# Optimization experiments

Measured on AMD Instinct MI355X. Metric: run time of the kernel, lower is better.

## Reference

```python
import jax, jax.numpy as jnp
import numpy as np

N, E, D, H, C, HOPS = 50000, 1600000, 128, 4, 32, 3

def spectral_normalize(W, iters=5):
    # power iteration, fixed start vector (deterministic, jit-friendly)
    u = jnp.ones((W.shape[0],), W.dtype) / jnp.sqrt(jnp.float32(W.shape[0]))
    for _ in range(iters):
        v = W.T @ u; v = v / (jnp.linalg.norm(v) + 1e-12)
        u = W @ v;  u = u / (jnp.linalg.norm(u) + 1e-12)
    sigma = u @ (W @ v)
    return W / (sigma + 1e-12)

def layer_norm(x, g, b, eps=1e-5):
    m = jnp.mean(x, -1, keepdims=True)
    v = jnp.mean((x - m) ** 2, -1, keepdims=True)
    return (x - m) * jax.lax.rsqrt(v + eps) * g + b

def edge_softmax(logits, dst):
    # logits: [E, H]; softmax over edges sharing a destination node
    m = jax.ops.segment_max(logits, dst, num_segments=N)
    e = jnp.exp(logits - m[dst])
    s = jax.ops.segment_sum(e, dst, num_segments=N)
    return e / (s[dst] + 1e-16)

def gat_layer(h, src, dst, W, a_s, a_d, bias):
    xh = (h @ W).reshape(N, H, C)                      # [N,H,C]
    al_s = jnp.sum(xh * a_s, -1)                       # [N,H]
    al_d = jnp.sum(xh * a_d, -1)
    logits = jax.nn.leaky_relu(al_s[src] + al_d[dst], 0.2)  # [E,H]
    alpha = edge_softmax(logits, dst)                  # [E,H]
    msg = xh[src] * alpha[..., None]                   # [E,H,C]
    out = jax.ops.segment_sum(msg, dst, num_segments=N)
    return out.reshape(N, H * C) + bias

def ode_block(h, W_ode, b_ode, steps=4):
    # fixed-step RK4 over t in [0,1]; f(h) = gelu(h @ sn(W) + b)
    Wn = spectral_normalize(W_ode)
    f = lambda y: jax.nn.gelu(y @ Wn + b_ode, approximate=False)
    dt = 1.0 / steps
    def step(y, _):
        k1 = f(y); k2 = f(y + 0.5 * dt * k1)
        k3 = f(y + 0.5 * dt * k2); k4 = f(y + dt * k3)
        return y + (dt / 6.0) * (k1 + 2 * k2 + 2 * k3 + k4), None
    y, _ = jax.lax.scan(step, h, None, length=steps)
    return y

def multihop_broadcast(h, src, dst, att):
    deg = jnp.maximum(jax.ops.segment_sum(jnp.ones((E,), h.dtype), dst, num_segments=N), 1.0)
    hops = [h]
    cur = h
    for _ in range(HOPS):
        cur = jax.ops.segment_sum(cur[src], dst, num_segments=N) / deg[:, None]
        hops.append(cur)
    stack = jnp.stack(hops)                            # [HOPS+1, N, D]
    scores = jnp.einsum('knd,d->kn', stack, att)       # [HOPS+1, N]
    w = jax.nn.softmax(scores, axis=0)
    return jnp.einsum('kn,knd->nd', w, stack)

def encoder_fwd(x, edge_index, W_in, b_in, W1, a_src1, a_dst1, b1,
                W2, a_src2, a_dst2, b2, g1, be1, g2, be2, W_ode, b_ode, att):
    src, dst = edge_index[0], edge_index[1]
    h = jax.nn.gelu(x @ spectral_normalize(W_in) + b_in, approximate=False)
    h = layer_norm(jax.nn.gelu(gat_layer(h, src, dst, W1, a_src1, a_dst1, b1), approximate=False), g1, be1)
    h = layer_norm(jax.nn.gelu(gat_layer(h, src, dst, W2, a_src2, a_dst2, b2), approximate=False), g2, be2)
    h = ode_block(h, W_ode, b_ode)
    h = multihop_broadcast(h, src, dst, att)
    return h

def setup_inputs() -> dict:
    key = jax.random.key(0)
    ks = jax.random.split(key, 12)
    s = lambda d: 1.0 / np.sqrt(d)
    return {
        'x': jax.random.normal(ks[0], (N, D), jnp.float32),
        'edge_index': jax.random.randint(ks[1], (2, E), 0, N, jnp.int64),
        'W_in': jax.random.normal(ks[2], (D, D), jnp.float32) * s(D),
        'b_in': jnp.zeros((D,), jnp.float32),
        'W1': jax.random.normal(ks[3], (D, H * C), jnp.float32) * s(D),
        'a_src1': jax.random.normal(ks[4], (H, C), jnp.float32) * s(C),
        'a_dst1': jax.random.normal(ks[5], (H, C), jnp.float32) * s(C),
        'b1': jnp.zeros((H * C,), jnp.float32),
        'W2': jax.random.normal(ks[6], (D, H * C), jnp.float32) * s(D),
        'a_src2': jax.random.normal(ks[7], (H, C), jnp.float32) * s(C),
        'a_dst2': jax.random.normal(ks[8], (H, C), jnp.float32) * s(C),
        'b2': jnp.zeros((H * C,), jnp.float32),
        'g1': jnp.ones((D,), jnp.float32), 'be1': jnp.zeros((D,), jnp.float32),
        'g2': jnp.ones((D,), jnp.float32), 'be2': jnp.zeros((D,), jnp.float32),
        'W_ode': jax.random.normal(ks[9], (D, D), jnp.float32) * s(D),
        'b_ode': jnp.zeros((D,), jnp.float32),
        'att': jax.random.normal(ks[10], (D,), jnp.float32) * s(D),
    }

def reference(x, edge_index, W_in, b_in, W1, a_src1, a_dst1, b1, W2, a_src2, a_dst2, b2,
              g1, be1, g2, be2, W_ode, b_ode, att):
    return encoder_fwd(x, edge_index, W_in, b_in, W1, a_src1, a_dst1, b1,
                       W2, a_src2, a_dst2, b2, g1, be1, g2, be2, W_ode, b_ode, att)
```

## Files before the change

kernel.cpp:

```cpp
#include <hip/hip_runtime.h>
#include <math.h>


typedef __attribute__((ext_vector_type(8))) short bf16x8;
typedef __attribute__((ext_vector_type(4))) float f32x4;

#define BSN 256

__device__ __forceinline__ float gelu_f(float x) {
    return 0.5f * x * (1.0f + erff(x * 0.70710678118654752f));
}
__device__ __forceinline__ float gelu_sig(float x) {
    float y = 0.7978845608028654f * fmaf(0.044715f * x, x * x, x);
    float e = __expf(-2.0f * y);
    return x * __builtin_amdgcn_rcpf(1.0f + e);
}
__device__ __forceinline__ unsigned pack_bf16(float a, float b) {
    unsigned ua = __float_as_uint(a), ub = __float_as_uint(b);
    ua += 0x7fffu + ((ua >> 16) & 1u);
    ub += 0x7fffu + ((ub >> 16) & 1u);
    return (ua >> 16) | (ub & 0xffff0000u);
}
__device__ __forceinline__ unsigned short bfbits(float x) {
    unsigned u = __float_as_uint(x);
    u += 0x7fffu + ((u >> 16) & 1u);
    return (unsigned short)(u >> 16);
}
__device__ __forceinline__ float bf_lo(unsigned u) { return __uint_as_float(u << 16); }
__device__ __forceinline__ float bf_hi(unsigned u) { return __uint_as_float(u & 0xffff0000u); }
__device__ __forceinline__ int swz(int byte) { return byte ^ (((byte >> 8) & 15) << 4); }

__launch_bounds__(128, 1)
__global__ void sn_k(const float* __restrict__ Win, const float* __restrict__ Wode,
                     float* __restrict__ WnIn, float* __restrict__ WnOde)
{
    __shared__ float Ws[128 * 128];
    __shared__ float Wt[128 * 128];
    __shared__ float red[128];
    const float* W  = (blockIdx.x == 0) ? Win  : Wode;
    float*       Wn = (blockIdx.x == 0) ? WnIn : WnOde;
    const int t = threadIdx.x;

    for (int i = t * 4; i < 16384; i += 512) {
        float4 v = *(const float4*)&W[i];
        *(float4*)&Ws[i] = v;
        int r = i >> 7, c = i & 127;
        Wt[(c + 0) * 128 + r] = v.x;
        Wt[(c + 1) * 128 + r] = v.y;
        Wt[(c + 2) * 128 + r] = v.z;
        Wt[(c + 3) * 128 + r] = v.w;
    }
    __syncthreads();

    float u = 0.088388347648318447f;
    float v = 0.0f;
    for (int it = 0; it < 5; it++) {
        red[t] = u; __syncthreads();
        float vv = 0.f;
        for (int i = 0; i < 128; i++) vv = fmaf(Ws[i * 128 + t], red[i], vv);
        __syncthreads();
        red[t] = vv * vv; __syncthreads();
        for (int s = 64; s > 0; s >>= 1) { if (t < s) red[t] += red[t + s]; __syncthreads(); }
        float nv = sqrtf(red[0]) + 1e-12f;
        v = vv / nv;
        __syncthreads();
        red[t] = v; __syncthreads();
        float uu = 0.f;
        for (int i = 0; i < 128; i++) uu = fmaf(Wt[i * 128 + t], red[i], uu);
        __syncthreads();
        red[t] = uu * uu; __syncthreads();
        for (int s = 64; s > 0; s >>= 1) { if (t < s) red[t] += red[t + s]; __syncthreads(); }
        float nu = sqrtf(red[0]) + 1e-12f;
        u = uu / nu;
        __syncthreads();
    }
    red[t] = v; __syncthreads();
    float wv = 0.f;
    for (int i = 0; i < 128; i++) wv = fmaf(Wt[i * 128 + t], red[i], wv);
    __syncthreads();
    red[t] = u * wv; __syncthreads();
    for (int s = 64; s > 0; s >>= 1) { if (t < s) red[t] += red[t + s]; __syncthreads(); }
    float inv = 1.0f / (red[0] + 1e-12f);
    __syncthreads();
    for (int i = t * 4; i < 16384; i += 512) {
        float4 w = *(const float4*)&Ws[i];
        w.x *= inv; w.y *= inv; w.z *= inv; w.w *= inv;
        *(float4*)&Wn[i] = w;
    }
}

__global__ void hist_k(const int* __restrict__ dst, int* __restrict__ deg, int E, int N)
{
    int e = blockIdx.x * blockDim.x + threadIdx.x;
    if (e < E) {
        int d = dst[e];
        d = (d < 0) ? 0 : (d >= N ? N - 1 : d);
        atomicAdd(&deg[d], 1);
    }
}

__launch_bounds__(1024, 1)
__global__ void scan_k(const int* __restrict__ deg, int* __restrict__ offs, int n)
{
    __shared__ int part[1024];
    const int t = threadIdx.x;
    const int chunk = (n + 1023) >> 10;
    int lo = t * chunk; if (lo > n) lo = n;
    int hi = lo + chunk; if (hi > n) hi = n;
    int s = 0;
    for (int i = lo; i < hi; i++) s += deg[i];
    part[t] = s; __syncthreads();
    for (int d = 1; d < 1024; d <<= 1) {
        int v = (t >= d) ? part[t - d] : 0;
        __syncthreads();
        part[t] += v;
        __syncthreads();
    }
    int run = (t == 0) ? 0 : part[t - 1];
    for (int i = lo; i < hi; i++) { offs[i] = run; run += deg[i]; }
    if (t == 1023) offs[n] = run;
}

__global__ void binit_k(const int* __restrict__ offs, int* __restrict__ bcur, int N, int nb)
{
    int b = blockIdx.x * blockDim.x + threadIdx.x;
    if (b < nb) {
        int n = b * BSN; if (n > N) n = N;
        bcur[b] = offs[n];
    }
}

__launch_bounds__(256, 2)
__global__ void scatA_k(const int* __restrict__ src, const int* __restrict__ dst,
                        int* __restrict__ bcur, uint2* __restrict__ pairbuf, int E, int N)
{
    __shared__ int cnt[256];
    __shared__ int sc[256];
    __shared__ int ebase[256];
    __shared__ int delta[256];
    __shared__ uint2 pr[4096];
    __shared__ unsigned char bid[4096];
    const int t = threadIdx.x;
    const int e0 = blockIdx.x * 4096;

    int s[16], d[16], rk[16], bb[16];
    cnt[t] = 0;
    __syncthreads();
#pragma unroll
    for (int i = 0; i < 16; i++) {
        int e = e0 + i * 256 + t;
        if (e < E) {
            int dd = dst[e]; dd = (dd < 0) ? 0 : (dd >= N ? N - 1 : dd);
            int ss = src[e]; ss = (ss < 0) ? 0 : (ss >= N ? N - 1 : ss);
            s[i] = ss; d[i] = dd; bb[i] = dd >> 8;
            rk[i] = atomicAdd(&cnt[bb[i]], 1);
        } else bb[i] = -1;
    }
    __syncthreads();
    sc[t] = cnt[t]; __syncthreads();
    for (int st = 1; st < 256; st <<= 1) {
        int v = (t >= st) ? sc[t - st] : 0;
        __syncthreads();
        sc[t] += v;
        __syncthreads();
    }
    int excl = sc[t] - cnt[t];
    int gbase = (cnt[t] > 0) ? atomicAdd(&bcur[t], cnt[t]) : 0;
    ebase[t] = excl;
    delta[t] = gbase - excl;
    __syncthreads();
#pragma unroll
    for (int i = 0; i < 16; i++) {
        if (bb[i] >= 0) {
            int slot = ebase[bb[i]] + rk[i];
            pr[slot] = make_uint2((unsigned)s[i], (unsigned)d[i]);
            bid[slot] = (unsigned char)bb[i];
        }
    }
    __syncthreads();
    const int total = sc[255];
    for (int i2 = t; i2 < total; i2 += 256) {
        int b = bid[i2];
        pairbuf[delta[b] + i2] = pr[i2];
    }
}

__launch_bounds__(256, 4)
__global__ void scatB_k(const uint2* __restrict__ pairbuf, const int* __restrict__ offs,
                        int* __restrict__ col, int N)
{
    __shared__ int cur[BSN];
    const int b = blockIdx.x;
    const int n0 = b * BSN;
    const int t = threadIdx.x;
    int nn = N - n0; if (nn > BSN) nn = BSN;
    if (t < nn) cur[t] = offs[n0 + t];
    __syncthreads();
    const int es = offs[n0], ee = offs[n0 + nn];
    for (int e = es + t; e < ee; e += 256) {
        uint2 p = pairbuf[e];
        int pos = atomicAdd(&cur[(int)p.y - n0], 1);
        col[pos] = (int)p.x;
    }
}

__launch_bounds__(256, 2)
__global__ void gemm_mfma_k(const float* __restrict__ in, const float* __restrict__ W,
                            const float* __restrict__ bias, float* __restrict__ out_f32,
                            unsigned short* __restrict__ out_bf, int nrows, int mode,
                            const float* __restrict__ a_s, const float* __restrict__ a_d,
                            float* __restrict__ als, float* __restrict__ ald)
{
    __shared__ unsigned short Wt[128 * 128];
    __shared__ unsigned short As[128 * 128];
    const int t = threadIdx.x;
    const int w = t >> 6, lane = t & 63;
    const int cl = lane & 15, lg = lane >> 4;
    const int r0 = blockIdx.x * 128;

    for (int i = t; i < 16384; i += 256) {
        int k = i >> 7, c = i & 127;
        *(unsigned short*)((char*)Wt + swz((c << 8) + (k << 1))) = bfbits(W[i]);
    }
    for (int i2 = t; i2 < 4096; i2 += 256) {
        int r = i2 >> 5, k0 = (i2 & 31) * 4;
        int rc = r0 + r; if (rc > nrows - 1) rc = nrows - 1;
        float4 v = *(const float4*)&in[(size_t)rc * 128 + k0];
        *(uint2*)((char*)As + swz((r << 8) + (k0 << 1))) =
            make_uint2(pack_bf16(v.x, v.y), pack_bf16(v.z, v.w));
    }
    __syncthreads();

    bf16x8 af[2][4];
#pragma unroll
    for (int rt = 0; rt < 2; rt++)
#pragma unroll
        for (int ks = 0; ks < 4; ks++)
            af[rt][ks] = *(const bf16x8*)((char*)As +
                           swz((w * 32 + rt * 16 + cl) * 256 + ks * 64 + lg * 16));

    f32x4 acc[2][8];
#pragma unroll
    for (int rt = 0; rt < 2; rt++)
#pragma unroll
        for (int n = 0; n < 8; n++) acc[rt][n] = (f32x4){0.f, 0.f, 0.f, 0.f};

#pragma unroll
    for (int n = 0; n < 8; n++) {
#pragma unroll
        for (int ks = 0; ks < 4; ks++) {
            bf16x8 bf = *(const bf16x8*)((char*)Wt +
                          swz((n * 16 + cl) * 256 + ks * 64 + lg * 16));
            acc[0][n] = __builtin_amdgcn_mfma_f32_16x16x32_bf16(af[0][ks], bf, acc[0][n], 0, 0, 0);
            acc[1][n] = __builtin_amdgcn_mfma_f32_16x16x32_bf16(af[1][ks], bf, acc[1][n], 0, 0, 0);
        }
    }

    if (mode == 0) {
        float asv[4][2], adv[4][2];
#pragma unroll
        for (int h = 0; h < 4; h++) {
            asv[h][0] = a_s[h * 32 + cl];      asv[h][1] = a_s[h * 32 + 16 + cl];
            adv[h][0] = a_d[h * 32 + cl];      adv[h][1] = a_d[h * 32 + 16 + cl];
        }
#pragma unroll
        for (int rt = 0; rt < 2; rt++) {
#pragma unroll
            for (int q = 0; q < 4; q++) {
                int row = r0 + w * 32 + rt * 16 + lg * 4 + q;
                float sh[4], dh[4];
#pragma unroll
                for (int h = 0; h < 4; h++) {
                    sh[h] = acc[rt][2 * h][q] * asv[h][0] + acc[rt][2 * h + 1][q] * asv[h][1];
                    dh[h] = acc[rt][2 * h][q] * adv[h][0] + acc[rt][2 * h + 1][q] * adv[h][1];
                }
#pragma unroll
                for (int mk = 1; mk < 16; mk <<= 1) {
#pragma unroll
                    for (int h = 0; h < 4; h++) {
                        sh[h] += __shfl_xor(sh[h], mk);
                        dh[h] += __shfl_xor(dh[h], mk);
                    }
                }
                if (cl == 0 && row < nrows) {
#pragma unroll
                    for (int h = 0; h < 4; h++) {
                        als[(size_t)row * 4 + h] = sh[h];
                        ald[(size_t)row * 4 + h] = dh[h];
                    }
                }
            }
#pragma unroll
            for (int q = 0; q < 4; q++) {
                int row = r0 + w * 32 + rt * 16 + lg * 4 + q;
                if (row < nrows) {
#pragma unroll
                    for (int n = 0; n < 8; n++)
                        out_bf[(size_t)row * 128 + n * 16 + cl] = bfbits(acc[rt][n][q]);
                }
            }
        }
    } else {
        float bc[8];
#pragma unroll
        for (int n = 0; n < 8; n++) bc[n] = bias[n * 16 + cl];
#pragma unroll
        for (int rt = 0; rt < 2; rt++)
#pragma unroll
            for (int q = 0; q < 4; q++) {
                int row = r0 + w * 32 + rt * 16 + lg * 4 + q;
                if (row < nrows) {
#pragma unroll
                    for (int n = 0; n < 8; n++)
                        out_f32[(size_t)row * 128 + n * 16 + cl] =
                            gelu_f(acc[rt][n][q] + bc[n]);
                }
            }
    }
}

__launch_bounds__(256)
__global__ void gat_agg2_k(const unsigned* __restrict__ xhbf, const float* __restrict__ als,
                           const float* __restrict__ ald, const int* __restrict__ col,
                           const int* __restrict__ offs, const float* __restrict__ bias,
                           const float* __restrict__ g, const float* __restrict__ be,
                           float* __restrict__ hout, int nnodes)
{
    __shared__ float alph[8][32][4];
    __shared__ int   scol[8][32];
    const int gq = threadIdx.x >> 5;
    const int n = blockIdx.x * 8 + gq;
    if (n >= nnodes) return;
    const int l = threadIdx.x & 31;
    const int e0 = offs[n], e1 = offs[n + 1];
    const float4 aldv = *(const float4*)&ald[(size_t)n * 4];

    float m0 = -1e30f, m1 = -1e30f, m2 = -1e30f, m3 = -1e30f;
    float s0 = 0.f, s1 = 0.f, s2 = 0.f, s3 = 0.f;
    for (int i = e0 + l; i < e1; i += 32) {
        int sv = col[i];
        float4 av = *(const float4*)&als[(size_t)sv * 4];
        float l0 = av.x + aldv.x; l0 = l0 > 0.f ? l0 : 0.2f * l0;
        float l1 = av.y + aldv.y; l1 = l1 > 0.f ? l1 : 0.2f * l1;
        float l2 = av.z + aldv.z; l2 = l2 > 0.f ? l2 : 0.2f * l2;
        float l3 = av.w + aldv.w; l3 = l3 > 0.f ? l3 : 0.2f * l3;
        float M;
        M = fmaxf(m0, l0); s0 = s0 * __expf(m0 - M) + __expf(l0 - M); m0 = M;
        M = fmaxf(m1, l1); s1 = s1 * __expf(m1 - M) + __expf(l1 - M); m1 = M;
        M = fmaxf(m2, l2); s2 = s2 * __expf(m2 - M) + __expf(l2 - M); m2 = M;
        M = fmaxf(m3, l3); s3 = s3 * __expf(m3 - M) + __expf(l3 - M); m3 = M;
    }
#pragma unroll
    for (int mk = 1; mk < 32; mk <<= 1) {
        float mo, so, M;
        mo = __shfl_xor(m0, mk); so = __shfl_xor(s0, mk);
        M = fmaxf(m0, mo); s0 = s0 * __expf(m0 - M) + so * __expf(mo - M); m0 = M;
        mo = __shfl_xor(m1, mk); so = __shfl_xor(s1, mk);
        M = fmaxf(m1, mo); s1 = s1 * __expf(m1 - M) + so * __expf(mo - M); m1 = M;
        mo = __shfl_xor(m2, mk); so = __shfl_xor(s2, mk);
        M = fmaxf(m2, mo); s2 = s2 * __expf(m2 - M) + so * __expf(mo - M); m2 = M;
        mo = __shfl_xor(m3, mk); so = __shfl_xor(s3, mk);
        M = fmaxf(m3, mo); s3 = s3 * __expf(m3 - M) + so * __expf(mo - M); m3 = M;
    }
    const float i0 = 1.f / (s0 + 1e-16f), i1 = 1.f / (s1 + 1e-16f);
    const float i2 = 1.f / (s2 + 1e-16f), i3 = 1.f / (s3 + 1e-16f);

    const int hh = l >> 3;
    float a0 = 0.f, a1 = 0.f, a2 = 0.f, a3 = 0.f;
    for (int base = e0; base < e1; base += 32) {
        int idx = base + l;
        if (idx < e1) {
            int sv = col[idx];
            float4 av = *(const float4*)&als[(size_t)sv * 4];
            float l0 = av.x + aldv.x; l0 = l0 > 0.f ? l0 : 0.2f * l0;
            float l1 = av.y + aldv.y; l1 = l1 > 0.f ? l1 : 0.2f * l1;
            float l2 = av.z + aldv.z; l2 = l2 > 0.f ? l2 : 0.2f * l2;
            float l3 = av.w + aldv.w; l3 = l3 > 0.f ? l3 : 0.2f * l3;
            float4 a4;
            a4.x = __expf(l0 - m0) * i0;
            a4.y = __expf(l1 - m1) * i1;
            a4.z = __expf(l2 - m2) * i2;
            a4.w = __expf(l3 - m3) * i3;
            *(float4*)&alph[gq][l][0] = a4;
            scol[gq][l] = sv;
        }
        int cnt = e1 - base; if (cnt > 32) cnt = 32;
#pragma unroll 4
        for (int j = 0; j < cnt; j++) {
            int sj = scol[gq][j];
            float aj = alph[gq][j][hh];
            uint2 u = *(const uint2*)&xhbf[(size_t)sj * 64 + l * 2];
            a0 = fmaf(aj, bf_lo(u.x), a0);
            a1 = fmaf(aj, bf_hi(u.x), a1);
            a2 = fmaf(aj, bf_lo(u.y), a2);
            a3 = fmaf(aj, bf_hi(u.y), a3);
        }
    }

    const int c0 = l * 4;
    float4 bv = *(const float4*)&bias[c0];
    float v0 = gelu_f(a0 + bv.x);
    float v1 = gelu_f(a1 + bv.y);
    float v2 = gelu_f(a2 + bv.z);
    float v3 = gelu_f(a3 + bv.w);
    float sum = v0 + v1 + v2 + v3;
#pragma unroll
    for (int mk = 1; mk < 32; mk <<= 1) sum += __shfl_xor(sum, mk);
    float mean = sum * (1.0f / 128.0f);
    float d0 = v0 - mean, d1 = v1 - mean, d2 = v2 - mean, d3 = v3 - mean;
    float vs = d0 * d0 + d1 * d1 + d2 * d2 + d3 * d3;
#pragma unroll
    for (int mk = 1; mk < 32; mk <<= 1) vs += __shfl_xor(vs, mk);
    float rstd = rsqrtf(vs * (1.0f / 128.0f) + 1e-5f);
    float4 gv = *(const float4*)&g[c0];
    float4 ev = *(const float4*)&be[c0];
    float4 o;
    o.x = d0 * rstd * gv.x + ev.x;
    o.y = d1 * rstd * gv.y + ev.y;
    o.z = d2 * rstd * gv.z + ev.z;
    o.w = d3 * rstd * gv.w + ev.w;
    *(float4*)&hout[(size_t)n * 128 + c0] = o;
}

__launch_bounds__(512, 2)
__global__ void ode_mfma_k(const float* __restrict__ yin, const float* __restrict__ Wn,
                           const float* __restrict__ bias, unsigned short* __restrict__ ybf,
                           int nrows, int nchunks)
{
    __shared__ unsigned short Wt[128 * 128];
    __shared__ unsigned short tl[4][2][16 * 128];
    const int t = threadIdx.x;
    const int w = t >> 6, lane = t & 63;
    const int pair = w >> 1, hf = w & 1;
    const int cl = lane & 15, lg = lane >> 4;

    for (int i = t; i < 16384; i += 512) {
        int k = i >> 7, c = i & 127;
        *(unsigned short*)((char*)Wt + swz((c << 8) + (k << 1))) = bfbits(Wn[i]);
    }

    float bcol[4];
#pragma unroll
    for (int n = 0; n < 4; n++) bcol[n] = bias[(hf * 4 + n) * 16 + cl];

    int radr[4], badr[4][4], wadr[4][4];
#pragma unroll
    for (int ks = 0; ks < 4; ks++)
        radr[ks] = swz(cl * 256 + ks * 64 + lg * 16);
#pragma unroll
    for (int n = 0; n < 4; n++) {
#pragma unroll
        for (int ks = 0; ks < 4; ks++)
            badr[n][ks] = swz(((hf * 4 + n) * 16 + cl) * 256 + ks * 64 + lg * 16);
#pragma unroll
        for (int q = 0; q < 4; q++)
            wadr[n][q] = swz((lg * 4 + q) * 256 + ((hf * 4 + n) * 16 + cl) * 2);
    }

    const float dt = 0.25f;
    char* tb0 = (char*)&tl[pair][0][0];
    char* tb1 = (char*)&tl[pair][1][0];

    int chunk = blockIdx.x * 4 + pair;
    if (chunk > nchunks - 1) chunk = nchunks - 1;
    const int r0 = chunk * 16;

    for (int i2 = hf * 64 + lane; i2 < 512; i2 += 128) {
        int r = i2 >> 5, k0 = (i2 & 31) * 4;
        int rc = r0 + r; if (rc > nrows - 1) rc = nrows - 1;
        float4 v = *(const float4*)&yin[(size_t)rc * 128 + k0];
        *(uint2*)(tb0 + swz(r * 256 + k0 * 2)) =
            make_uint2(pack_bf16(v.x, v.y), pack_bf16(v.z, v.w));
    }
    float yv[4][4], av[4][4];
#pragma unroll
    for (int q = 0; q < 4; q++) {
        int rc = r0 + lg * 4 + q; if (rc > nrows - 1) rc = nrows - 1;
        const float* rp = &yin[(size_t)rc * 128 + hf * 64 + cl];
#pragma unroll
        for (int n = 0; n < 4; n++) { yv[n][q] = rp[n * 16]; av[n][q] = yv[n][q]; }
    }
    __syncthreads();

    char* pc = tb0;
    char* pn = tb1;
#pragma unroll 1
    for (int step = 0; step < 4; step++) {
#pragma unroll 1
        for (int st = 0; st < 4; st++) {
            const float ca = (st == 0 || st == 3) ? dt / 6.f : dt / 3.f;
            const float ct = (st < 2) ? dt * 0.5f : dt;
            const bool last = (st == 3);
            bf16x8 af[4];
#pragma unroll
            for (int ks = 0; ks < 4; ks++)
                af[ks] = *(const bf16x8*)(pc + radr[ks]);
            f32x4 acc[4];
#pragma unroll
            for (int n = 0; n < 4; n++) {
                acc[n] = (f32x4){0.f, 0.f, 0.f, 0.f};
#pragma unroll
                for (int ks = 0; ks < 4; ks++) {
                    bf16x8 bf = *(const bf16x8*)((char*)Wt + badr[n][ks]);
                    acc[n] = __builtin_amdgcn_mfma_f32_16x16x32_bf16(af[ks], bf, acc[n], 0, 0, 0);
                }
            }
#pragma unroll
            for (int n = 0; n < 4; n++) {
#pragma unroll
                for (int q = 0; q < 4; q++) {
                    float kk = gelu_sig(acc[n][q] + bcol[n]);
                    av[n][q] = fmaf(ca, kk, av[n][q]);
                    float tn;
                    if (last) { yv[n][q] = av[n][q]; tn = av[n][q]; }
                    else      { tn = fmaf(ct, kk, yv[n][q]); }
                    *(unsigned short*)(pn + wadr[n][q]) = bfbits(tn);
                }
            }
            __syncthreads();
            char* tmp = pc; pc = pn; pn = tmp;
        }
    }
#pragma unroll
    for (int q = 0; q < 4; q++) {
        int rg = r0 + lg * 4 + q;
        if (rg < nrows) {
#pragma unroll
            for (int n = 0; n < 4; n++)
                ybf[(size_t)rg * 128 + hf * 64 + n * 16 + cl] = bfbits(av[n][q]);
        }
    }
}

__launch_bounds__(256)
__global__ void hop_k(const unsigned* __restrict__ cur, const int* __restrict__ col,
                      const int* __restrict__ offs, const int* __restrict__ deg,
                      unsigned* __restrict__ outbf, int nnodes)
{
    __shared__ int scol[8][32];
    const int gq = threadIdx.x >> 5;
    const int n = blockIdx.x * 8 + gq;
    if (n >= nnodes) return;
    const int l = threadIdx.x & 31;
    const int e0 = offs[n], e1 = offs[n + 1];
    float a0 = 0.f, a1 = 0.f, a2 = 0.f, a3 = 0.f;
    for (int base = e0; base < e1; base += 32) {
        int idx = base + l;
        if (idx < e1) scol[gq][l] = col[idx];
        int cnt = e1 - base; if (cnt > 32) cnt = 32;
#pragma unroll 4
        for (int j = 0; j < cnt; j++) {
            int sj = scol[gq][j];
            uint2 u = *(const uint2*)&cur[(size_t)sj * 64 + l * 2];
            a0 += bf_lo(u.x); a1 += bf_hi(u.x);
            a2 += bf_lo(u.y); a3 += bf_hi(u.y);
        }
    }
    float inv = 1.0f / fmaxf((float)deg[n], 1.0f);
    *(uint2*)&outbf[(size_t)n * 64 + l * 2] =
        make_uint2(pack_bf16(a0 * inv, a1 * inv), pack_bf16(a2 * inv, a3 * inv));
}

__launch_bounds__(256)
__global__ void final2_k(const unsigned* __restrict__ s0b, const unsigned* __restrict__ s1b,
                         const unsigned* __restrict__ s2b, const unsigned* __restrict__ s3b,
                         const float* __restrict__ att, float* __restrict__ outp, int nnodes)
{
    const int n = blockIdx.x * 4 + (threadIdx.x >> 6);
    if (n >= nnodes) return;
    const int lane = threadIdx.x & 63;
    size_t b = (size_t)n * 64 + lane;
    float2 a = *(const float2*)&att[lane * 2];
    unsigned u0 = s0b[b], u1 = s1b[b], u2 = s2b[b], u3 = s3b[b];
    float p0 = bf_lo(u0) * a.x + bf_hi(u0) * a.y;
    float p1 = bf_lo(u1) * a.x + bf_hi(u1) * a.y;
    float p2 = bf_lo(u2) * a.x + bf_hi(u2) * a.y;
    float p3 = bf_lo(u3) * a.x + bf_hi(u3) * a.y;
#pragma unroll
    for (int mk = 32; mk >= 1; mk >>= 1) {
        p0 += __shfl_xor(p0, mk); p1 += __shfl_xor(p1, mk);
        p2 += __shfl_xor(p2, mk); p3 += __shfl_xor(p3, mk);
    }
    float mm = fmaxf(fmaxf(p0, p1), fmaxf(p2, p3));
    float e0 = __expf(p0 - mm), e1 = __expf(p1 - mm), e2 = __expf(p2 - mm), e3 = __expf(p3 - mm);
    float inv = 1.0f / (e0 + e1 + e2 + e3);
    float w0 = e0 * inv, w1 = e1 * inv, w2 = e2 * inv, w3 = e3 * inv;
    float ox = w0 * bf_lo(u0) + w1 * bf_lo(u1) + w2 * bf_lo(u2) + w3 * bf_lo(u3);
    float oy = w0 * bf_hi(u0) + w1 * bf_hi(u1) + w2 * bf_hi(u2) + w3 * bf_hi(u3);
    *(float2*)&outp[(size_t)n * 128 + lane * 2] = make_float2(ox, oy);
}

extern "C" void kernel_launch(void* const* d_in, const int* in_sizes, int n_in,
                              void* d_out, int out_size, void* d_ws, size_t ws_size,
                              hipStream_t stream)
{
    const float* x     = (const float*)d_in[0];
    const int*   ei    = (const int*)d_in[1];
    const float* W_in  = (const float*)d_in[2];
    const float* b_in  = (const float*)d_in[3];
    const float* W1    = (const float*)d_in[4];
    const float* a_s1  = (const float*)d_in[5];
    const float* a_d1  = (const float*)d_in[6];
    const float* b1    = (const float*)d_in[7];
    const float* W2    = (const float*)d_in[8];
    const float* a_s2  = (const float*)d_in[9];
    const float* a_d2  = (const float*)d_in[10];
    const float* b2    = (const float*)d_in[11];
    const float* g1    = (const float*)d_in[12];
    const float* be1   = (const float*)d_in[13];
    const float* g2    = (const float*)d_in[14];
    const float* be2   = (const float*)d_in[15];
    const float* W_ode = (const float*)d_in[16];
    const float* b_ode = (const float*)d_in[17];
    const float* att   = (const float*)d_in[18];

    const int N = in_sizes[0] / 128;
    const int E = in_sizes[1] / 2;
    const int* srcv = ei;
    const int* dstv = ei + E;
    const int nb = (N + BSN - 1) / BSN;

    char* wsb = (char*)d_ws;
    size_t off = 0;
    auto alloc = [&](size_t bytes) -> void* {
        void* p = wsb + off;
        off = (off + bytes + 511) & ~(size_t)511;
        return p;
    };
    float*    WnIn   = (float*)alloc(65536);
    float*    WnOde  = (float*)alloc(65536);
    float*    als    = (float*)alloc((size_t)N * 4 * 4);
    float*    ald    = (float*)alloc((size_t)N * 4 * 4);
    int*      deg    = (int*)alloc((size_t)N * 4);
    int*      bcur   = (int*)alloc((size_t)(nb + 1) * 4);
    int*      offs   = (int*)alloc((size_t)(N + 1) * 4);
    int*      col    = (int*)alloc((size_t)E * 4);
    float*    B0     = (float*)alloc((size_t)N * 128 * 4);
    unsigned* xhbf   = (unsigned*)alloc((size_t)N * 64 * 4);
    unsigned* ybf    = (unsigned*)alloc((size_t)N * 64 * 4);
    unsigned* h2bf   = (unsigned*)alloc((size_t)N * 64 * 4);
    unsigned* h3bf   = (unsigned*)alloc((size_t)N * 64 * 4);
    uint2*    pairbuf = (uint2*)ybf;

    (void)hipMemsetAsync(deg, 0, (size_t)N * 4, stream);

    sn_k<<<2, 128, 0, stream>>>(W_in, W_ode, WnIn, WnOde);
    hist_k<<<(E + 255) / 256, 256, 0, stream>>>(dstv, deg, E, N);
    scan_k<<<1, 1024, 0, stream>>>(deg, offs, N);
    binit_k<<<(nb + 255) / 256, 256, 0, stream>>>(offs, bcur, N, nb);
    scatA_k<<<(E + 4095) / 4096, 256, 0, stream>>>(srcv, dstv, bcur, pairbuf, E, N);
    scatB_k<<<nb, 256, 0, stream>>>(pairbuf, offs, col, N);

    const int gblocks = (N + 127) / 128;
    const int ablocks = (N + 7) / 8;
    const int fblocks = (N + 3) / 4;

    gemm_mfma_k<<<gblocks, 256, 0, stream>>>(x, WnIn, b_in, B0, nullptr, N, 1,
        nullptr, nullptr, nullptr, nullptr);

    gemm_mfma_k<<<gblocks, 256, 0, stream>>>(B0, W1, nullptr, nullptr,
        (unsigned short*)xhbf, N, 0, a_s1, a_d1, als, ald);
    gat_agg2_k<<<ablocks, 256, 0, stream>>>(xhbf, als, ald, col, offs, b1, g1, be1, B0, N);

    gemm_mfma_k<<<gblocks, 256, 0, stream>>>(B0, W2, nullptr, nullptr,
        (unsigned short*)xhbf, N, 0, a_s2, a_d2, als, ald);
    gat_agg2_k<<<ablocks, 256, 0, stream>>>(xhbf, als, ald, col, offs, b2, g2, be2, B0, N);

    const int nchunks = (N + 15) / 16;
    const int oblocks = (nchunks + 3) / 4;
    ode_mfma_k<<<oblocks, 512, 0, stream>>>(B0, WnOde, b_ode, (unsigned short*)ybf, N, nchunks);

    hop_k<<<ablocks, 256, 0, stream>>>(ybf,  col, offs, deg, xhbf, N);
    hop_k<<<ablocks, 256, 0, stream>>>(xhbf, col, offs, deg, h2bf, N);
    hop_k<<<ablocks, 256, 0, stream>>>(h2bf, col, offs, deg, h3bf, N);
    final2_k<<<fblocks, 256, 0, stream>>>(ybf, xhbf, h2bf, h3bf, att, (float*)d_out, N);
}
```

Measured before the change: 663.7 us.

## Restructure ODE kernel to one chunk per block with register-resident weights

The RK4 ODE kernel now runs one 16-row chunk per 128-thread block instead of four chunks per 512-thread block. The weight B-fragments are loaded from LDS into registers once, removing repeated LDS reads of W inside the 16 RK stages. The tanh-approximation gelu is also algebraically folded to save a few flops. In exchange, each block rebuilds the bf16 weight tile in LDS, so W conversion and global traffic grow fourfold and the setup is spread over fewer threads.

Result: no change. 676.0 us (+1.9%).

```diff
diff --git a/kernel.cpp b/kernel.cpp
--- a/kernel.cpp
+++ b/kernel.cpp
@@ -11,8 +11,9 @@
     return 0.5f * x * (1.0f + erff(x * 0.70710678118654752f));
 }
 __device__ __forceinline__ float gelu_sig(float x) {
-    float y = 0.7978845608028654f * fmaf(0.044715f * x, x * x, x);
-    float e = __expf(-2.0f * y);
+    float x2 = x * x;
+    float f = fmaf(-0.0713548162f, x2, -1.5957691216f);
+    float e = __expf(x * f);
     return x * __builtin_amdgcn_rcpf(1.0f + e);
 }
 __device__ __forceinline__ unsigned pack_bf16(float a, float b) {
@@ -422,19 +423,18 @@
     *(float4*)&hout[(size_t)n * 128 + c0] = o;
 }
 
-__launch_bounds__(512, 2)
+__launch_bounds__(128, 2)
 __global__ void ode_mfma_k(const float* __restrict__ yin, const float* __restrict__ Wn,
                            const float* __restrict__ bias, unsigned short* __restrict__ ybf,
                            int nrows, int nchunks)
 {
     __shared__ unsigned short Wt[128 * 128];
-    __shared__ unsigned short tl[4][2][16 * 128];
+    __shared__ unsigned short tl[2][16 * 128];
     const int t = threadIdx.x;
-    const int w = t >> 6, lane = t & 63;
-    const int pair = w >> 1, hf = w & 1;
+    const int hf = t >> 6, lane = t & 63;
     const int cl = lane & 15, lg = lane >> 4;
 
-    for (int i = t; i < 16384; i += 512) {
+    for (int i = t; i < 16384; i += 128) {
         int k = i >> 7, c = i & 127;
         *(unsigned short*)((char*)Wt + swz((c << 8) + (k << 1))) = bfbits(Wn[i]);
     }
@@ -443,29 +443,25 @@
 #pragma unroll
     for (int n = 0; n < 4; n++) bcol[n] = bias[(hf * 4 + n) * 16 + cl];
 
-    int radr[4], badr[4][4], wadr[4][4];
+    int radr[4], wadr[4][4];
 #pragma unroll
     for (int ks = 0; ks < 4; ks++)
         radr[ks] = swz(cl * 256 + ks * 64 + lg * 16);
 #pragma unroll
-    for (int n = 0; n < 4; n++) {
-#pragma unroll
-        for (int ks = 0; ks < 4; ks++)
-            badr[n][ks] = swz(((hf * 4 + n) * 16 + cl) * 256 + ks * 64 + lg * 16);
+    for (int n = 0; n < 4; n++)
 #pragma unroll
         for (int q = 0; q < 4; q++)
             wadr[n][q] = swz((lg * 4 + q) * 256 + ((hf * 4 + n) * 16 + cl) * 2);
-    }
 
     const float dt = 0.25f;
-    char* tb0 = (char*)&tl[pair][0][0];
-    char* tb1 = (char*)&tl[pair][1][0];
-
-    int chunk = blockIdx.x * 4 + pair;
+    char* tb0 = (char*)&tl[0][0];
+    char* tb1 = (char*)&tl[1][0];
+
+    int chunk = blockIdx.x;
     if (chunk > nchunks - 1) chunk = nchunks - 1;
     const int r0 = chunk * 16;
 
-    for (int i2 = hf * 64 + lane; i2 < 512; i2 += 128) {
+    for (int i2 = t; i2 < 512; i2 += 128) {
         int r = i2 >> 5, k0 = (i2 & 31) * 4;
         int rc = r0 + r; if (rc > nrows - 1) rc = nrows - 1;
         float4 v = *(const float4*)&yin[(size_t)rc * 128 + k0];
@@ -481,6 +477,14 @@
         for (int n = 0; n < 4; n++) { yv[n][q] = rp[n * 16]; av[n][q] = yv[n][q]; }
     }
     __syncthreads();
+
+    bf16x8 bfr[4][4];
+#pragma unroll
+    for (int n = 0; n < 4; n++)
+#pragma unroll
+        for (int ks = 0; ks < 4; ks++)
+            bfr[n][ks] = *(const bf16x8*)((char*)Wt +
+                           swz(((hf * 4 + n) * 16 + cl) * 256 + ks * 64 + lg * 16));
 
     char* pc = tb0;
     char* pn = tb1;
@@ -500,10 +504,8 @@
             for (int n = 0; n < 4; n++) {
                 acc[n] = (f32x4){0.f, 0.f, 0.f, 0.f};
 #pragma unroll
-                for (int ks = 0; ks < 4; ks++) {
-                    bf16x8 bf = *(const bf16x8*)((char*)Wt + badr[n][ks]);
-                    acc[n] = __builtin_amdgcn_mfma_f32_16x16x32_bf16(af[ks], bf, acc[n], 0, 0, 0);
-                }
+                for (int ks = 0; ks < 4; ks++)
+                    acc[n] = __builtin_amdgcn_mfma_f32_16x16x32_bf16(af[ks], bfr[n][ks], acc[n], 0, 0, 0);
             }
 #pragma unroll
             for (int n = 0; n < 4; n++) {
@@ -667,8 +669,7 @@
     gat_agg2_k<<<ablocks, 256, 0, stream>>>(xhbf, als, ald, col, offs, b2, g2, be2, B0, N);
 
     const int nchunks = (N + 15) / 16;
-    const int oblocks = (nchunks + 3) / 4;
-    ode_mfma_k<<<oblocks, 512, 0, stream>>>(B0, WnOde, b_ode, (unsigned short*)ybf, N, nchunks);
+    ode_mfma_k<<<nchunks, 128, 0, stream>>>(B0, WnOde, b_ode, (unsigned short*)ybf, N, nchunks);
 
     hop_k<<<ablocks, 256, 0, stream>>>(ybf,  col, offs, deg, xhbf, N);
     hop_k<<<ablocks, 256, 0, stream>>>(xhbf, col, offs, deg, h2bf, N);
```
